# Kernel optimization log

Measured on AMD Instinct MI355X. Metric: run time of the kernel, lower is better.

## Reference

```python
import jax, jax.numpy as jnp
import numpy as np

BN_EPS = 1e-5


def setup_inputs() -> dict:
    key = jax.random.key(0)
    ks = jax.random.split(key, 8)
    B, C, T, H, W = 8, 64, 16, 56, 56
    Cr = C // 4  # ratio=4 bottleneck in RouteFuncMLP
    s = lambda k, shape, scale=0.05: jax.random.normal(k, shape, jnp.float32) * scale
    return {
        "x": jax.random.normal(ks[0], (B, C, T, H, W), jnp.float32),
        "view": 3,  # View.FOUL
        "emb": s(ks[1], (4, C), 1.0),
        "Wg": s(ks[2], (C, C)),
        "bg": jnp.zeros((C,), jnp.float32),
        "Wa": s(ks[3], (Cr, C, 3)),
        "ba": jnp.zeros((Cr,), jnp.float32),
        "bn_gamma": jnp.ones((Cr,), jnp.float32),
        "bn_beta": jnp.zeros((Cr,), jnp.float32),
        "bn_mean": jnp.zeros((Cr,), jnp.float32),
        "bn_var": jnp.ones((Cr,), jnp.float32),
        "Wb": s(ks[4], (C, Cr, 3)),
        "Wconv": s(ks[5], (C, C, 3, 3)),
        "Wcls": s(ks[6], (10, C)),
        "bcls": jnp.zeros((10,), jnp.float32),
    }


def _conv1d_t(x, w, pad):
    # Temporal conv: x [B, Cin, T], w [Cout, Cin, K] -> [B, Cout, T]
    return jax.lax.conv_general_dilated(
        x, w, window_strides=(1,), padding=[(pad, pad)],
        dimension_numbers=("NCH", "OIH", "NCH"))


def _route_func(x, Wg, bg, Wa, ba, bn_gamma, bn_beta, bn_mean, bn_var, Wb):
    # RouteFuncMLP: per-frame, per-channel calibration factors. x: [B,C,T,H,W]
    g = x.mean(axis=(2, 3, 4))  # global pool -> [B,C]
    xt = x.mean(axis=(3, 4))    # spatial pool -> [B,C,T]
    g = jnp.einsum("oc,bc->bo", Wg, g) + bg  # 1x1x1 conv on global branch
    h = _conv1d_t(xt + g[:, :, None], Wa, pad=1) + ba[None, :, None]  # [B,Cr,T]
    # BatchNorm3d (inference form with running stats)
    h = (h - bn_mean[None, :, None]) * jax.lax.rsqrt(bn_var[None, :, None] + BN_EPS)
    h = h * bn_gamma[None, :, None] + bn_beta[None, :, None]
    h = jax.nn.relu(h)
    return _conv1d_t(h, Wb, pad=1) + 1.0  # alpha: [B,C,T]


def reference(x, view, emb, Wg, bg, Wa, ba, bn_gamma, bn_beta, bn_mean, bn_var, Wb, Wconv, Wcls, bcls):
    B, C, T, H, W = x.shape
    # embed-add: broadcast the view embedding over T,H,W
    x = x + emb[view][None, :, None, None, None]
    alpha = _route_func(x, Wg, bg, Wa, ba, bn_gamma, bn_beta, bn_mean, bn_var, Wb)
    # TAdaConv2d with cal_dim='cin': scaling the shared kernel per input channel
    # (per batch, per frame) is mathematically identical to scaling the input
    # channels first and convolving with the shared kernel.
    xs = x * alpha[:, :, :, None, None]
    xs = xs.transpose(0, 2, 1, 3, 4).reshape(B * T, C, H, W)
    y = jax.lax.conv_general_dilated(
        xs, Wconv, window_strides=(1, 1), padding=[(1, 1), (1, 1)],
        dimension_numbers=("NCHW", "OIHW", "NCHW"))
    y = y.reshape(B, T, C, H, W).transpose(0, 2, 1, 3, 4)  # [B,C,T,H,W]
    pooled = y.max(axis=(2, 3, 4))  # max over T,H,W -> [B,C]
    return pooled @ Wcls.T + bcls   # [B,10]
```

## Files before the change

kernel.cpp:

```cpp
#include <hip/hip_runtime.h>
#include <math.h>

#define B_ 8
#define C_ 64
#define T_ 16
#define H_ 56
#define W_ 56
#define HW_ (H_ * W_)
#define CR_ 16
#define PLANE (T_ * HW_)

typedef __attribute__((ext_vector_type(8))) short bf16x8;
typedef __attribute__((ext_vector_type(4))) float f32x4;

__device__ __forceinline__ unsigned short f2bf(float f) {
    unsigned u = __float_as_uint(f);
    u += 0x7fffu + ((u >> 16) & 1u);
    return (unsigned short)(u >> 16);
}

__global__ __launch_bounds__(256) void prepack_kernel(
    const float* __restrict__ Wconv, unsigned short* __restrict__ packWbf)
{
    int idx = blockIdx.x * 256 + threadIdx.x;
    if (idx >= 64 * 576) return;
    int j     = idx & 7;
    int lane  = (idx >> 3) & 63;
    int mt    = (idx >> 9) & 3;
    int kstep = idx >> 11;
    int cih = kstep & 1, tap = kstep >> 1;
    int co = mt * 16 + (lane & 15);
    int ci = cih * 32 + (lane >> 4) * 8 + j;
    packWbf[idx] = f2bf(Wconv[(co * C_ + ci) * 9 + tap]);
}

__global__ __launch_bounds__(128) void pool_kernel(
    const float* __restrict__ x, float* __restrict__ xt)
{
    __shared__ float red[2];
    int bct = blockIdx.x;
    const float4* p = (const float4*)(x + (size_t)bct * HW_);
    int tid = threadIdx.x;
    float s = 0.f;
    #pragma unroll
    for (int k = 0; k < 7; ++k) {
        int i = tid + k * 128;
        if (i < 784) { float4 v = p[i]; s += (v.x + v.y) + (v.z + v.w); }
    }
    #pragma unroll
    for (int off = 32; off > 0; off >>= 1) s += __shfl_down(s, off);
    if ((tid & 63) == 0) red[tid >> 6] = s;
    __syncthreads();
    if (tid == 0) xt[bct] = red[0] + red[1];
}

__global__ __launch_bounds__(256) void route_kernel(
    const float* __restrict__ xt, const float* __restrict__ emb,
    const int* __restrict__ viewp,
    const float* __restrict__ Wg, const float* __restrict__ bg,
    const float* __restrict__ Wa, const float* __restrict__ ba,
    const float* __restrict__ bng, const float* __restrict__ bnb,
    const float* __restrict__ bnm, const float* __restrict__ bnv,
    const float* __restrict__ Wb, float* __restrict__ alphaT)
{
    __shared__ float swg[64 * 65];
    __shared__ float swa[64 * 49];
    __shared__ float swb[48 * 65];
    __shared__ float z[64 * 18];
    __shared__ float gs[64], ggs[64], sge[64];
    __shared__ float hs[16][18];
    int b = blockIdx.x, tid = threadIdx.x;

    if (tid < 64) sge[tid] = emb[viewp[0] * C_ + tid];
    for (int idx = tid; idx < 4096; idx += 256) {
        int c = idx >> 6, i = idx & 63;
        swg[c * 65 + i] = Wg[idx];
    }
    for (int idx = tid; idx < 3072; idx += 256) {
        float v = Wa[idx];
        int r = idx / 192, rem = idx - r * 192;
        int i = rem / 3, tap = rem - i * 3;
        swa[i * 49 + r * 3 + tap] = v;
    }
    for (int idx = tid; idx < 3072; idx += 256) {
        float v = Wb[idx];
        int c = idx / 48, k = idx - c * 48;
        swb[k * 65 + c] = v;
    }
    if (tid < 64) { z[tid * 18] = 0.f; z[tid * 18 + 17] = 0.f; }
    if (tid < 16) { hs[tid][0] = 0.f; hs[tid][17] = 0.f; }
    __syncthreads();
    for (int idx = tid; idx < 1024; idx += 256) {
        int c = idx >> 4, t = idx & 15;
        z[c * 18 + t + 1] = xt[b * 1024 + idx] * (1.f / HW_) + sge[c];
    }
    __syncthreads();

    if (tid < 64) {
        float s = 0.f;
        #pragma unroll
        for (int t = 1; t <= 16; ++t) s += z[tid * 18 + t];
        gs[tid] = s * (1.f / 16.f);
    }
    __syncthreads();
    if (tid < 64) {
        float acc = bg[tid];
        #pragma unroll 8
        for (int i = 0; i < 64; ++i) acc = fmaf(swg[tid * 65 + i], gs[i], acc);
        ggs[tid] = acc;
    }
    __syncthreads();
    for (int idx = tid; idx < 1024; idx += 256) {
        int c = idx >> 4, t = idx & 15;
        z[c * 18 + t + 1] += ggs[c];
    }
    __syncthreads();

    {
        int t = tid >> 4, r = tid & 15;
        float v = ba[r];
        #pragma unroll 8
        for (int i = 0; i < 64; ++i) {
            const float* wa = &swa[i * 49 + r * 3];
            const float* zz = &z[i * 18 + t];
            v = fmaf(zz[0], wa[0], v);
            v = fmaf(zz[1], wa[1], v);
            v = fmaf(zz[2], wa[2], v);
        }
        v = (v - bnm[r]) * rsqrtf(bnv[r] + 1e-5f);
        v = fmaf(v, bng[r], bnb[r]);
        hs[r][t + 1] = fmaxf(v, 0.f);
    }
    __syncthreads();

    for (int idx = tid; idx < 1024; idx += 256) {
        int t = idx >> 6, c = idx & 63;
        float v = 1.f;
        #pragma unroll
        for (int r = 0; r < 16; ++r) {
            v = fmaf(hs[r][t],     swb[(r * 3 + 0) * 65 + c], v);
            v = fmaf(hs[r][t + 1], swb[(r * 3 + 1) * 65 + c], v);
            v = fmaf(hs[r][t + 2], swb[(r * 3 + 2) * 65 + c], v);
        }
        alphaT[(b * T_ + t) * C_ + c] = v;
    }
}

#define LCOLS2 58
#define HROWE (4 * LCOLS2)

__global__ __launch_bounds__(256) void conv_mfma_kernel(
    const float* __restrict__ x, const float* __restrict__ emb,
    const int* __restrict__ viewp, const float* __restrict__ alphaT,
    const unsigned short* __restrict__ packWbf, float* __restrict__ part)
{
    __shared__ bf16x8 ltile[10 * HROWE];
    __shared__ float sa[C_], sea[C_];
    __shared__ float smax[4][C_];

    int blk = blockIdx.x;
    int strip = blk % 7;
    int bt = blk / 7;
    int b = bt >> 4, t = bt & 15;
    int h0 = strip * 8;
    int tid = threadIdx.x;
    int lane = tid & 63, wv = tid >> 6;
    int q = lane >> 4, li = lane & 15;

    if (tid < C_) {
        float a = alphaT[bt * C_ + tid];
        sa[tid] = a;
        sea[tid] = emb[viewp[0] * C_ + tid] * a;
    }
    if (tid >= 64 && tid < 144) {
        int i = tid - 64;
        int r = i / 8, c8 = i - r * 8;
        int ch4 = c8 >> 1, col = (c8 & 1) ? 57 : 0;
        ltile[(r * 4 + ch4) * LCOLS2 + col] = (bf16x8){0,0,0,0,0,0,0,0};
    }

    const float* xb = x + ((size_t)(b * C_) * T_ + t) * HW_;

    int baddr[7];
    #pragma unroll
    for (int nt = 0; nt < 7; ++nt) {
        int p = (wv * 7 + nt) * 16 + li;
        int row = p / W_, col = p - row * W_;
        baddr[nt] = row * HROWE + q * LCOLS2 + col;
    }

    f32x4 acc[7][4];
    #pragma unroll
    for (int nt = 0; nt < 7; ++nt)
        #pragma unroll
        for (int mt = 0; mt < 4; ++mt)
            acc[nt][mt] = (f32x4){0.f, 0.f, 0.f, 0.f};

    const bf16x8* pw = (const bf16x8*)packWbf;

    #pragma unroll
    for (int half = 0; half < 2; ++half) {
        __syncthreads();
        #pragma unroll
        for (int k = 0; k < 3; ++k) {
            int item = tid + k * 256;
            if (item < 560) {
                int ch4 = item / 140;
                int rem = item - ch4 * 140;
                int row = rem / 14, cq = rem - row * 14;
                int gr = h0 - 1 + row;
                int ci0 = half * 32 + ch4 * 8;
                bf16x8 hv[4] = {(bf16x8){0,0,0,0,0,0,0,0}, (bf16x8){0,0,0,0,0,0,0,0},
                                (bf16x8){0,0,0,0,0,0,0,0}, (bf16x8){0,0,0,0,0,0,0,0}};
                if ((unsigned)gr < (unsigned)H_) {
                    const float* src = xb + (size_t)ci0 * PLANE + gr * W_ + cq * 4;
                    float4 f[8];
                    #pragma unroll
                    for (int j = 0; j < 8; ++j)
                        f[j] = *(const float4*)(src + (size_t)j * PLANE);
                    #pragma unroll
                    for (int j = 0; j < 8; ++j) {
                        float aj = sa[ci0 + j], ej = sea[ci0 + j];
                        hv[0][j] = (short)f2bf(fmaf(f[j].x, aj, ej));
                        hv[1][j] = (short)f2bf(fmaf(f[j].y, aj, ej));
                        hv[2][j] = (short)f2bf(fmaf(f[j].z, aj, ej));
                        hv[3][j] = (short)f2bf(fmaf(f[j].w, aj, ej));
                    }
                }
                bf16x8* dst = &ltile[(row * 4 + ch4) * LCOLS2 + cq * 4 + 1];
                #pragma unroll
                for (int cc = 0; cc < 4; ++cc) dst[cc] = hv[cc];
            }
        }
        __syncthreads();

        #pragma unroll
        for (int tap = 0; tap < 9; ++tap) {
            const int kh = tap / 3, kw = tap % 3;
            const int kstep = tap * 2 + half;
            const int boff = kh * HROWE + kw;
            bf16x8 af[4];
            #pragma unroll
            for (int mt = 0; mt < 4; ++mt)
                af[mt] = pw[(kstep * 4 + mt) * 64 + lane];
            #pragma unroll
            for (int nt = 0; nt < 7; ++nt) {
                bf16x8 bfr = ltile[baddr[nt] + boff];
                #pragma unroll
                for (int mt = 0; mt < 4; ++mt)
                    acc[nt][mt] = __builtin_amdgcn_mfma_f32_16x16x32_bf16(
                        af[mt], bfr, acc[nt][mt], 0, 0, 0);
            }
        }
    }

    float m[4][4];
    #pragma unroll
    for (int mt = 0; mt < 4; ++mt)
        #pragma unroll
        for (int i = 0; i < 4; ++i) {
            float v = acc[0][mt][i];
            #pragma unroll
            for (int nt = 1; nt < 7; ++nt) v = fmaxf(v, acc[nt][mt][i]);
            m[mt][i] = v;
        }
    #pragma unroll
    for (int off = 1; off < 16; off <<= 1)
        #pragma unroll
        for (int mt = 0; mt < 4; ++mt)
            #pragma unroll
            for (int i = 0; i < 4; ++i)
                m[mt][i] = fmaxf(m[mt][i], __shfl_xor(m[mt][i], off));
    if (li == 0) {
        #pragma unroll
        for (int mt = 0; mt < 4; ++mt)
            #pragma unroll
            for (int i = 0; i < 4; ++i)
                smax[wv][mt * 16 + q * 4 + i] = m[mt][i];
    }
    __syncthreads();
    if (tid < C_) {
        float mm = fmaxf(fmaxf(smax[0][tid], smax[1][tid]),
                         fmaxf(smax[2][tid], smax[3][tid]));
        part[(size_t)blk * C_ + tid] = mm;
    }
}

__global__ __launch_bounds__(512) void cls_kernel(
    const float* __restrict__ part, const float* __restrict__ Wcls,
    const float* __restrict__ bcls, float* __restrict__ out)
{
    __shared__ float pooled[512];
    int tid = threadIdx.x;
    int b = tid >> 6, c = tid & 63;
    const float* pb = part + (size_t)b * 112 * C_ + c;
    float m0 = -INFINITY, m1 = -INFINITY, m2 = -INFINITY, m3 = -INFINITY;
    #pragma unroll
    for (int i = 0; i < 28; ++i) {
        m0 = fmaxf(m0, pb[(i     ) * C_]);
        m1 = fmaxf(m1, pb[(i + 28) * C_]);
        m2 = fmaxf(m2, pb[(i + 56) * C_]);
        m3 = fmaxf(m3, pb[(i + 84) * C_]);
    }
    pooled[tid] = fmaxf(fmaxf(m0, m1), fmaxf(m2, m3));
    __syncthreads();
    if (tid < B_ * 10) {
        int bb = tid / 10, k = tid - (tid / 10) * 10;
        float v = bcls[k];
        #pragma unroll 8
        for (int cc = 0; cc < C_; ++cc)
            v = fmaf(pooled[bb * C_ + cc], Wcls[k * C_ + cc], v);
        out[tid] = v;
    }
}

extern "C" void kernel_launch(void* const* d_in, const int* in_sizes, int n_in,
                              void* d_out, int out_size, void* d_ws, size_t ws_size,
                              hipStream_t stream)
{
    const float* x     = (const float*)d_in[0];
    const int*   view  = (const int*)  d_in[1];
    const float* emb   = (const float*)d_in[2];
    const float* Wg    = (const float*)d_in[3];
    const float* bg    = (const float*)d_in[4];
    const float* Wa    = (const float*)d_in[5];
    const float* ba    = (const float*)d_in[6];
    const float* bng   = (const float*)d_in[7];
    const float* bnb   = (const float*)d_in[8];
    const float* bnm   = (const float*)d_in[9];
    const float* bnv   = (const float*)d_in[10];
    const float* Wb    = (const float*)d_in[11];
    const float* Wconv = (const float*)d_in[12];
    const float* Wcls  = (const float*)d_in[13];
    const float* bcls  = (const float*)d_in[14];
    float* out = (float*)d_out;

    char* wsb = (char*)d_ws;
    float*          xt      = (float*)(wsb + 0);
    float*          alphaT  = (float*)(wsb + 32768);
    float*          part    = (float*)(wsb + 65536);
    unsigned short* packWbf = (unsigned short*)(wsb + 294912);

    hipLaunchKernelGGL(prepack_kernel, dim3(144), dim3(256), 0, stream,
                       Wconv, packWbf);
    hipLaunchKernelGGL(pool_kernel, dim3(B_ * C_ * T_), dim3(128), 0, stream,
                       x, xt);
    hipLaunchKernelGGL(route_kernel, dim3(B_), dim3(256), 0, stream,
                       xt, emb, view, Wg, bg, Wa, ba, bng, bnb, bnm, bnv, Wb, alphaT);
    hipLaunchKernelGGL(conv_mfma_kernel, dim3(B_ * T_ * 7), dim3(256), 0, stream,
                       x, emb, view, alphaT, packWbf, part);
    hipLaunchKernelGGL(cls_kernel, dim3(1), dim3(512), 0, stream,
                       part, Wcls, bcls, out);
}
```

Measured before the change: 90.16 us.

## Fuse prepack into pool kernel and recompute route MLP inside conv blocks

Weight prepacking now runs as extra blocks of the pooling kernel, and the single-block-per-batch route kernel is removed. Each conv block instead redundantly recomputes the route MLP for its own frame, using LDS scratch aliased onto the tile buffer. This cuts two kernel launches and the serial low-occupancy route stage. The cost is extra per-block prologue work and more global reads of the weight tensors across 896 blocks.

```diff
diff --git a/kernel.cpp b/kernel.cpp
--- a/kernel.cpp
+++ b/kernel.cpp
@@ -19,28 +19,28 @@
     return (unsigned short)(u >> 16);
 }
 
-__global__ __launch_bounds__(256) void prepack_kernel(
-    const float* __restrict__ Wconv, unsigned short* __restrict__ packWbf)
+__global__ __launch_bounds__(128) void pool_prepack_kernel(
+    const float* __restrict__ x, const float* __restrict__ Wconv,
+    float* __restrict__ xt, unsigned short* __restrict__ packWbf)
 {
-    int idx = blockIdx.x * 256 + threadIdx.x;
-    if (idx >= 64 * 576) return;
-    int j     = idx & 7;
-    int lane  = (idx >> 3) & 63;
-    int mt    = (idx >> 9) & 3;
-    int kstep = idx >> 11;
-    int cih = kstep & 1, tap = kstep >> 1;
-    int co = mt * 16 + (lane & 15);
-    int ci = cih * 32 + (lane >> 4) * 8 + j;
-    packWbf[idx] = f2bf(Wconv[(co * C_ + ci) * 9 + tap]);
-}
-
-__global__ __launch_bounds__(128) void pool_kernel(
-    const float* __restrict__ x, float* __restrict__ xt)
-{
+    int blk = blockIdx.x;
+    int tid = threadIdx.x;
+    if (blk >= 8192) {
+        int idx = (blk - 8192) * 128 + tid;
+        if (idx < 64 * 576) {
+            int j     = idx & 7;
+            int lane  = (idx >> 3) & 63;
+            int mt    = (idx >> 9) & 3;
+            int kstep = idx >> 11;
+            int cih = kstep & 1, tap = kstep >> 1;
+            int co = mt * 16 + (lane & 15);
+            int ci = cih * 32 + (lane >> 4) * 8 + j;
+            packWbf[idx] = f2bf(Wconv[(co * C_ + ci) * 9 + tap]);
+        }
+        return;
+    }
     __shared__ float red[2];
-    int bct = blockIdx.x;
-    const float4* p = (const float4*)(x + (size_t)bct * HW_);
-    int tid = threadIdx.x;
+    const float4* p = (const float4*)(x + (size_t)blk * HW_);
     float s = 0.f;
     #pragma unroll
     for (int k = 0; k < 7; ++k) {
@@ -51,107 +51,20 @@
     for (int off = 32; off > 0; off >>= 1) s += __shfl_down(s, off);
     if ((tid & 63) == 0) red[tid >> 6] = s;
     __syncthreads();
-    if (tid == 0) xt[bct] = red[0] + red[1];
-}
-
-__global__ __launch_bounds__(256) void route_kernel(
-    const float* __restrict__ xt, const float* __restrict__ emb,
-    const int* __restrict__ viewp,
+    if (tid == 0) xt[blk] = red[0] + red[1];
+}
+
+#define LCOLS2 58
+#define HROWE (4 * LCOLS2)
+
+__global__ __launch_bounds__(256) void conv_mfma_kernel(
+    const float* __restrict__ x, const float* __restrict__ emb,
+    const int* __restrict__ viewp, const float* __restrict__ xt,
     const float* __restrict__ Wg, const float* __restrict__ bg,
     const float* __restrict__ Wa, const float* __restrict__ ba,
     const float* __restrict__ bng, const float* __restrict__ bnb,
     const float* __restrict__ bnm, const float* __restrict__ bnv,
-    const float* __restrict__ Wb, float* __restrict__ alphaT)
-{
-    __shared__ float swg[64 * 65];
-    __shared__ float swa[64 * 49];
-    __shared__ float swb[48 * 65];
-    __shared__ float z[64 * 18];
-    __shared__ float gs[64], ggs[64], sge[64];
-    __shared__ float hs[16][18];
-    int b = blockIdx.x, tid = threadIdx.x;
-
-    if (tid < 64) sge[tid] = emb[viewp[0] * C_ + tid];
-    for (int idx = tid; idx < 4096; idx += 256) {
-        int c = idx >> 6, i = idx & 63;
-        swg[c * 65 + i] = Wg[idx];
-    }
-    for (int idx = tid; idx < 3072; idx += 256) {
-        float v = Wa[idx];
-        int r = idx / 192, rem = idx - r * 192;
-        int i = rem / 3, tap = rem - i * 3;
-        swa[i * 49 + r * 3 + tap] = v;
-    }
-    for (int idx = tid; idx < 3072; idx += 256) {
-        float v = Wb[idx];
-        int c = idx / 48, k = idx - c * 48;
-        swb[k * 65 + c] = v;
-    }
-    if (tid < 64) { z[tid * 18] = 0.f; z[tid * 18 + 17] = 0.f; }
-    if (tid < 16) { hs[tid][0] = 0.f; hs[tid][17] = 0.f; }
-    __syncthreads();
-    for (int idx = tid; idx < 1024; idx += 256) {
-        int c = idx >> 4, t = idx & 15;
-        z[c * 18 + t + 1] = xt[b * 1024 + idx] * (1.f / HW_) + sge[c];
-    }
-    __syncthreads();
-
-    if (tid < 64) {
-        float s = 0.f;
-        #pragma unroll
-        for (int t = 1; t <= 16; ++t) s += z[tid * 18 + t];
-        gs[tid] = s * (1.f / 16.f);
-    }
-    __syncthreads();
-    if (tid < 64) {
-        float acc = bg[tid];
-        #pragma unroll 8
-        for (int i = 0; i < 64; ++i) acc = fmaf(swg[tid * 65 + i], gs[i], acc);
-        ggs[tid] = acc;
-    }
-    __syncthreads();
-    for (int idx = tid; idx < 1024; idx += 256) {
-        int c = idx >> 4, t = idx & 15;
-        z[c * 18 + t + 1] += ggs[c];
-    }
-    __syncthreads();
-
-    {
-        int t = tid >> 4, r = tid & 15;
-        float v = ba[r];
-        #pragma unroll 8
-        for (int i = 0; i < 64; ++i) {
-            const float* wa = &swa[i * 49 + r * 3];
-            const float* zz = &z[i * 18 + t];
-            v = fmaf(zz[0], wa[0], v);
-            v = fmaf(zz[1], wa[1], v);
-            v = fmaf(zz[2], wa[2], v);
-        }
-        v = (v - bnm[r]) * rsqrtf(bnv[r] + 1e-5f);
-        v = fmaf(v, bng[r], bnb[r]);
-        hs[r][t + 1] = fmaxf(v, 0.f);
-    }
-    __syncthreads();
-
-    for (int idx = tid; idx < 1024; idx += 256) {
-        int t = idx >> 6, c = idx & 63;
-        float v = 1.f;
-        #pragma unroll
-        for (int r = 0; r < 16; ++r) {
-            v = fmaf(hs[r][t],     swb[(r * 3 + 0) * 65 + c], v);
-            v = fmaf(hs[r][t + 1], swb[(r * 3 + 1) * 65 + c], v);
-            v = fmaf(hs[r][t + 2], swb[(r * 3 + 2) * 65 + c], v);
-        }
-        alphaT[(b * T_ + t) * C_ + c] = v;
-    }
-}
-
-#define LCOLS2 58
-#define HROWE (4 * LCOLS2)
-
-__global__ __launch_bounds__(256) void conv_mfma_kernel(
-    const float* __restrict__ x, const float* __restrict__ emb,
-    const int* __restrict__ viewp, const float* __restrict__ alphaT,
+    const float* __restrict__ Wb,
     const unsigned short* __restrict__ packWbf, float* __restrict__ part)
 {
     __shared__ bf16x8 ltile[10 * HROWE];
@@ -165,13 +78,91 @@
     int h0 = strip * 8;
     int tid = threadIdx.x;
     int lane = tid & 63, wv = tid >> 6;
-    int q = lane >> 4, li = lane & 15;
-
-    if (tid < C_) {
-        float a = alphaT[bt * C_ + tid];
-        sa[tid] = a;
-        sea[tid] = emb[viewp[0] * C_ + tid] * a;
-    }
+    int q4 = lane >> 4, li = lane & 15;
+
+    float* scr = (float*)ltile;
+    float* z   = scr;
+    float* swa = scr + 1152;
+    float* hsv = scr + 4288;
+    float* ggv = scr + 4352;
+    float* gsv = scr + 4416;
+
+    {
+        int view = viewp[0];
+        for (int i = tid; i < 1024; i += 256) {
+            int c = i >> 4, tt = i & 15;
+            z[c * 18 + tt + 1] = xt[b * 1024 + i] * (1.f / HW_) + emb[view * C_ + c];
+        }
+        if (tid < 128) { int c = tid & 63; z[c * 18 + (tid < 64 ? 0 : 17)] = 0.f; }
+        for (int i = tid; i < 3072; i += 256) {
+            float v = Wa[i];
+            int r = i / 192, rem = i - r * 192;
+            int ii = rem / 3, tap = rem - ii * 3;
+            swa[ii * 49 + r * 3 + tap] = v;
+        }
+    }
+    __syncthreads();
+    if (tid < 64) {
+        float s = 0.f;
+        #pragma unroll
+        for (int k = 1; k <= 16; ++k) s += z[tid * 18 + k];
+        gsv[tid] = s * (1.f / 16.f);
+    }
+    __syncthreads();
+    {
+        float p = 0.f;
+        const float* wrow = Wg + tid * 16;
+        int q = tid & 3;
+        #pragma unroll
+        for (int k = 0; k < 16; ++k) p = fmaf(wrow[k], gsv[q * 16 + k], p);
+        p += __shfl_xor(p, 1);
+        p += __shfl_xor(p, 2);
+        if (q == 0) ggv[tid >> 2] = p + bg[tid >> 2];
+    }
+    __syncthreads();
+    for (int i = tid; i < 1024; i += 256) {
+        int c = i >> 4, tt = i & 15;
+        z[c * 18 + tt + 1] += ggv[c];
+    }
+    __syncthreads();
+    if (tid < 48) {
+        int r = tid & 15, s = tid >> 4;
+        int tp = t - 1 + s;
+        float hv = 0.f;
+        if ((unsigned)tp < 16u) {
+            float v = ba[r];
+            #pragma unroll 8
+            for (int i2 = 0; i2 < 64; ++i2) {
+                const float* wa = swa + i2 * 49 + r * 3;
+                const float* zr = z + i2 * 18 + tp;
+                v = fmaf(zr[0], wa[0], v);
+                v = fmaf(zr[1], wa[1], v);
+                v = fmaf(zr[2], wa[2], v);
+            }
+            v = (v - bnm[r]) * rsqrtf(bnv[r] + 1e-5f);
+            v = fmaf(v, bng[r], bnb[r]);
+            hv = fmaxf(v, 0.f);
+        }
+        hsv[r * 3 + s] = hv;
+    }
+    __syncthreads();
+    {
+        float p = 0.f;
+        const float* wrow = Wb + tid * 12;
+        int q = tid & 3;
+        #pragma unroll
+        for (int k = 0; k < 12; ++k) p = fmaf(wrow[k], hsv[q * 12 + k], p);
+        p += __shfl_xor(p, 1);
+        p += __shfl_xor(p, 2);
+        if (q == 0) {
+            int c = tid >> 2;
+            float a = p + 1.f;
+            sa[c] = a;
+            sea[c] = emb[viewp[0] * C_ + c] * a;
+        }
+    }
+    __syncthreads();
+
     if (tid >= 64 && tid < 144) {
         int i = tid - 64;
         int r = i / 8, c8 = i - r * 8;
@@ -186,7 +177,7 @@
     for (int nt = 0; nt < 7; ++nt) {
         int p = (wv * 7 + nt) * 16 + li;
         int row = p / W_, col = p - row * W_;
-        baddr[nt] = row * HROWE + q * LCOLS2 + col;
+        baddr[nt] = row * HROWE + q4 * LCOLS2 + col;
     }
 
     f32x4 acc[7][4];
@@ -276,7 +267,7 @@
         for (int mt = 0; mt < 4; ++mt)
             #pragma unroll
             for (int i = 0; i < 4; ++i)
-                smax[wv][mt * 16 + q * 4 + i] = m[mt][i];
+                smax[wv][mt * 16 + q4 * 4 + i] = m[mt][i];
     }
     __syncthreads();
     if (tid < C_) {
@@ -337,18 +328,14 @@
 
     char* wsb = (char*)d_ws;
     float*          xt      = (float*)(wsb + 0);
-    float*          alphaT  = (float*)(wsb + 32768);
-    float*          part    = (float*)(wsb + 65536);
-    unsigned short* packWbf = (unsigned short*)(wsb + 294912);
-
-    hipLaunchKernelGGL(prepack_kernel, dim3(144), dim3(256), 0, stream,
-                       Wconv, packWbf);
-    hipLaunchKernelGGL(pool_kernel, dim3(B_ * C_ * T_), dim3(128), 0, stream,
-                       x, xt);
-    hipLaunchKernelGGL(route_kernel, dim3(B_), dim3(256), 0, stream,
-                       xt, emb, view, Wg, bg, Wa, ba, bng, bnb, bnm, bnv, Wb, alphaT);
+    float*          part    = (float*)(wsb + 32768);
+    unsigned short* packWbf = (unsigned short*)(wsb + 262144);
+
+    hipLaunchKernelGGL(pool_prepack_kernel, dim3(8192 + 288), dim3(128), 0, stream,
+                       x, Wconv, xt, packWbf);
     hipLaunchKernelGGL(conv_mfma_kernel, dim3(B_ * T_ * 7), dim3(256), 0, stream,
-                       x, emb, view, alphaT, packWbf, part);
+                       x, emb, view, xt, Wg, bg, Wa, ba, bng, bnb, bnm, bnv, Wb,
+                       packWbf, part);
     hipLaunchKernelGGL(cls_kernel, dim3(1), dim3(512), 0, stream,
                        part, Wcls, bcls, out);
 }
```

After: 82.52 us. 1.09x faster.
